# Optimization experiments

Measured on AMD Instinct MI355X. Metric: run time of the kernel, lower is better.

## Reference

```python
import jax, jax.numpy as jnp
import numpy as np

# Hyperparameters mirroring init_kwargs
MAX_ITERS = 100      # ADMM outer iterations
RHO = 1.0            # ADMM penalty
INNER = 20           # PGD steps per x-subproblem
STEP = 5e-05         # fixed PGD step (x_inner_step given, so no svdvals branch)


def setup_inputs() -> dict:
    key = jax.random.key(0)
    kA, kb, kc = jax.random.split(key, 3)
    m, n = 2048, 4096
    A = jax.random.normal(kA, (m, n), dtype=jnp.float32)
    b = jax.random.uniform(kb, (m,), dtype=jnp.float32)
    c = jax.random.uniform(kc, (n,), dtype=jnp.float32)
    return {"A": A, "b": b, "c": c}


def _admm(A, b, c):
    m, n = A.shape

    def outer(carry, _):
        x, s, u = carry
        r = s + b - u  # target for the x-subproblem residual

        # PGD on: min_{x>=0} c^T x + (rho/2)||A x - r||^2
        def pgd(x, _):
            g = c + RHO * (A.T @ (A @ x - r))
            return jnp.maximum(x - STEP * g, 0.0), None

        x, _ = jax.lax.scan(pgd, x, None, length=INNER)

        Ax = A @ x
        s = jnp.maximum(Ax - b + u, 0.0)   # slack update (projection onto >=0)
        u = u + (Ax - s - b)               # scaled dual update
        return (x, s, u), None

    init = (jnp.zeros((n,), A.dtype), jnp.zeros((m,), A.dtype), jnp.zeros((m,), A.dtype))
    (x, s, u), _ = jax.lax.scan(outer, init, None, length=MAX_ITERS)
    lambda_kkt = -RHO * u
    return x, s, u, lambda_kkt


def reference(A, b, c):
    # return_history=False -> torch module returns (x, s, u, lambda_kkt, None);
    # we return the 4 tensor outputs.
    return _admm(A, b, c)
```

## Files before the change

### kernel.cpp

```cpp
#include <hip/hip_runtime.h>
#include <hip/hip_cooperative_groups.h>

namespace cg = cooperative_groups;
typedef unsigned int u32;
typedef unsigned long long u64;

#define M_ROWS 2048
#define N_COLS 4096
#define RHO_C 1.0f
#define STEP_C 5e-05f
#define MAX_ITERS_C 100
#define INNER_C 20

__device__ __forceinline__ u64 ald64(const u64* p) {
    return __hip_atomic_load(p, __ATOMIC_RELAXED, __HIP_MEMORY_SCOPE_AGENT);
}
__device__ __forceinline__ void ast64(u64* p, u64 v) {
    __hip_atomic_store(p, v, __ATOMIC_RELAXED, __HIP_MEMORY_SCOPE_AGENT);
}
__device__ __forceinline__ void push_slot(u64* p, float v, u32 tag) {
    ast64(p, ((u64)tag << 32) | (u64)__float_as_uint(v));
}
__device__ __forceinline__ float4 poll4(const u64* p, u32 tag) {
    for (;;) {
        u64 a = ald64(p),     b = ald64(p + 1);
        u64 c = ald64(p + 2), d = ald64(p + 3);
        if (((u32)(a >> 32) == tag) & ((u32)(b >> 32) == tag) &
            ((u32)(c >> 32) == tag) & ((u32)(d >> 32) == tag))
            return make_float4(__uint_as_float((u32)a), __uint_as_float((u32)b),
                               __uint_as_float((u32)c), __uint_as_float((u32)d));
        __builtin_amdgcn_s_sleep(1);
    }
}
__device__ __forceinline__ float2 poll2(const u64* p, u32 tag) {
    for (;;) {
        u64 a = ald64(p), b = ald64(p + 1);
        if (((u32)(a >> 32) == tag) & ((u32)(b >> 32) == tag))
            return make_float2(__uint_as_float((u32)a), __uint_as_float((u32)b));
        __builtin_amdgcn_s_sleep(1);
    }
}

__global__ __launch_bounds__(1024) void admm_push(
    const float* __restrict__ A, const float* __restrict__ bvec,
    const float* __restrict__ cvec, float* __restrict__ out,
    u64* __restrict__ xmb, u64* __restrict__ rmb, int fanout)
{
    const int tid  = threadIdx.x;
    const int blk  = blockIdx.x;
    const int lane = tid & 63;
    const int wave = tid >> 6;
    const int cgp  = wave >> 2;
    const int rq   = wave & 3;
    const int cpy  = (fanout == 1) ? 0 : (blk & 7);

    __shared__ float  abuf[4 * N_COLS];
    __shared__ float4 xs4[1024];
    __shared__ float  red[4][16];
    __shared__ float4 gred[64];
    __shared__ float  wl[16], cw[16];
    __shared__ float  sv[8], uv[8], tpart[16], rtnew[8];

    float* xs = reinterpret_cast<float*>(xs4);
    const float4* A4 = reinterpret_cast<const float4*>(A);
    float4* abuf4 = reinterpret_cast<float4*>(abuf);
    const u64* xmyc = xmb + (size_t)cpy * 8192;
    const u64* rmyc = rmb + (size_t)cpy * 4096;

    if (tid < 16) cw[tid] = cvec[blk * 16 + tid];
    if (tid < 8) { sv[tid] = 0.0f; uv[tid] = 0.0f; }

    float accM[4][16];
    #pragma unroll
    for (int r = 0; r < 4; ++r)
        #pragma unroll
        for (int k = 0; k < 16; ++k) accM[r][k] = 0.0f;

    for (int i0 = 0; i0 < M_ROWS; i0 += 4) {
        #pragma unroll
        for (int ii = 0; ii < 4; ++ii)
            abuf4[ii * 1024 + tid] = A4[(size_t)(i0 + ii) * 1024 + tid];
        __syncthreads();
        #pragma unroll
        for (int ii = 0; ii < 4; ++ii) {
            const float*  row  = abuf + ii * N_COLS;
            const float4* row4 = abuf4 + ii * 1024;
            float4 av[4];
            #pragma unroll
            for (int q = 0; q < 4; ++q)
                av[q] = row4[256 * cgp + 64 * q + lane];
            float cb[4];
            #pragma unroll
            for (int r = 0; r < 4; ++r) cb[r] = row[blk * 16 + rq * 4 + r];
            #pragma unroll
            for (int r = 0; r < 4; ++r)
                #pragma unroll
                for (int q = 0; q < 4; ++q) {
                    accM[r][4*q+0] = fmaf(cb[r], av[q].x, accM[r][4*q+0]);
                    accM[r][4*q+1] = fmaf(cb[r], av[q].y, accM[r][4*q+1]);
                    accM[r][4*q+2] = fmaf(cb[r], av[q].z, accM[r][4*q+2]);
                    accM[r][4*q+3] = fmaf(cb[r], av[q].w, accM[r][4*q+3]);
                }
        }
        __syncthreads();
    }

    for (int outer = 0; outer < MAX_ITERS_C; ++outer) {
        if (outer == 0) {
            abuf[2 * tid]     = bvec[2 * tid];
            abuf[2 * tid + 1] = bvec[2 * tid + 1];
        } else {
            float2 rv = poll2(rmyc + (outer & 1) * 2048 + 2 * tid, (u32)outer);
            abuf[2 * tid]     = rv.x;
            abuf[2 * tid + 1] = rv.y;
        }
        __syncthreads();

        {
            const int p = tid >> 2, gq = tid & 3;
            float4 acc = {0.f, 0.f, 0.f, 0.f};
            #pragma unroll
            for (int k2 = 0; k2 < 8; ++k2) {
                const int i = p + 256 * k2;
                const float tv = abuf[i];
                float4 a = A4[(size_t)i * 1024 + blk * 4 + gq];
                acc.x = fmaf(a.x, tv, acc.x); acc.y = fmaf(a.y, tv, acc.y);
                acc.z = fmaf(a.z, tv, acc.z); acc.w = fmaf(a.w, tv, acc.w);
            }
            #pragma unroll
            for (int off = 4; off < 64; off <<= 1) {
                acc.x += __shfl_xor(acc.x, off);
                acc.y += __shfl_xor(acc.y, off);
                acc.z += __shfl_xor(acc.z, off);
                acc.w += __shfl_xor(acc.w, off);
            }
            if ((lane >> 2) == 0) gred[wave * 4 + gq] = acc;
        }
        __syncthreads();
        if (tid < 4) {
            float4 tot = {0.f, 0.f, 0.f, 0.f};
            #pragma unroll
            for (int w = 0; w < 16; ++w) {
                float4 v = gred[w * 4 + tid];
                tot.x += v.x; tot.y += v.y; tot.z += v.z; tot.w += v.w;
            }
            wl[tid * 4 + 0] = tot.x; wl[tid * 4 + 1] = tot.y;
            wl[tid * 4 + 2] = tot.z; wl[tid * 4 + 3] = tot.w;
        }
        __syncthreads();

        for (int inner = 0; inner < INNER_C; ++inner) {
            const u32 gs = (u32)(outer * INNER_C + inner);

            if (gs == 0) {
                xs4[tid] = make_float4(0.f, 0.f, 0.f, 0.f);
                __syncthreads();
            } else if (inner > 0) {
                float4 xv = poll4(xmyc + (gs & 1) * 4096 + 4 * tid, gs);
                __syncthreads();
                xs4[tid] = xv;
                __syncthreads();
            }

            float4 xq[4];
            #pragma unroll
            for (int q = 0; q < 4; ++q)
                xq[q] = xs4[256 * cgp + 64 * q + lane];

            float4 pd = {0.f, 0.f, 0.f, 0.f};
            #pragma unroll
            for (int q = 0; q < 4; ++q) {
                pd.x = fmaf(accM[0][4*q+0], xq[q].x, pd.x);
                pd.x = fmaf(accM[0][4*q+1], xq[q].y, pd.x);
                pd.x = fmaf(accM[0][4*q+2], xq[q].z, pd.x);
                pd.x = fmaf(accM[0][4*q+3], xq[q].w, pd.x);
                pd.y = fmaf(accM[1][4*q+0], xq[q].x, pd.y);
                pd.y = fmaf(accM[1][4*q+1], xq[q].y, pd.y);
                pd.y = fmaf(accM[1][4*q+2], xq[q].z, pd.y);
                pd.y = fmaf(accM[1][4*q+3], xq[q].w, pd.y);
                pd.z = fmaf(accM[2][4*q+0], xq[q].x, pd.z);
                pd.z = fmaf(accM[2][4*q+1], xq[q].y, pd.z);
                pd.z = fmaf(accM[2][4*q+2], xq[q].z, pd.z);
                pd.z = fmaf(accM[2][4*q+3], xq[q].w, pd.z);
                pd.w = fmaf(accM[3][4*q+0], xq[q].x, pd.w);
                pd.w = fmaf(accM[3][4*q+1], xq[q].y, pd.w);
                pd.w = fmaf(accM[3][4*q+2], xq[q].z, pd.w);
                pd.w = fmaf(accM[3][4*q+3], xq[q].w, pd.w);
            }
            #pragma unroll
            for (int off = 32; off; off >>= 1) {
                pd.x += __shfl_xor(pd.x, off);
                pd.y += __shfl_xor(pd.y, off);
                pd.z += __shfl_xor(pd.z, off);
                pd.w += __shfl_xor(pd.w, off);
            }
            if (lane == 0) {
                red[cgp][rq * 4 + 0] = pd.x;
                red[cgp][rq * 4 + 1] = pd.y;
                red[cgp][rq * 4 + 2] = pd.z;
                red[cgp][rq * 4 + 3] = pd.w;
            }
            __syncthreads();

            if (tid < fanout * 16) {
                const int dst = tid >> 4, jj = tid & 15;
                const float y = red[0][jj] + red[1][jj]
                              + red[2][jj] + red[3][jj];
                const float g = cw[jj] + RHO_C * (y - wl[jj]);
                float xn = xs[blk * 16 + jj] - STEP_C * g;
                xn = xn > 0.f ? xn : 0.f;
                push_slot(xmb + (size_t)dst * 8192 + ((gs + 1) & 1) * 4096
                              + blk * 16 + jj, xn, gs + 1);
            }
        }

        {
            const u32 gsf = (u32)((outer + 1) * INNER_C);
            float4 xv = poll4(xmyc + (gsf & 1) * 4096 + 4 * tid, gsf);
            __syncthreads();
            xs4[tid] = xv;
            __syncthreads();
        }
        {
            const int r = blk * 8 + (wave >> 1), h = wave & 1;
            const float4* Ar = A4 + (size_t)r * 1024 + h * 512;
            const float4* xh = xs4 + h * 512;
            float4 acc = {0.f, 0.f, 0.f, 0.f};
            #pragma unroll
            for (int it = 0; it < 8; ++it) {
                float4 a = Ar[it * 64 + lane], xv = xh[it * 64 + lane];
                acc.x = fmaf(a.x, xv.x, acc.x); acc.y = fmaf(a.y, xv.y, acc.y);
                acc.z = fmaf(a.z, xv.z, acc.z); acc.w = fmaf(a.w, xv.w, acc.w);
            }
            float d = acc.x + acc.y + acc.z + acc.w;
            #pragma unroll
            for (int off = 32; off; off >>= 1) d += __shfl_xor(d, off);
            if (lane == 0) tpart[wave] = d;
        }
        __syncthreads();
        if (tid < 8) {
            const int i = blk * 8 + tid;
            const float a  = tpart[2 * tid] + tpart[2 * tid + 1];
            const float bb = bvec[i];
            const float uu = uv[tid];
            float sn = a - bb + uu; sn = sn > 0.f ? sn : 0.f;
            const float un = uu + a - sn - bb;
            sv[tid] = sn; uv[tid] = un;
            rtnew[tid] = sn + bb - un;
        }
        __syncthreads();
        if (tid < fanout * 8) {
            const int dst = tid >> 3, jj = tid & 7;
            push_slot(rmb + (size_t)dst * 4096 + ((outer + 1) & 1) * 2048
                          + blk * 8 + jj, rtnew[jj], (u32)(outer + 1));
        }
    }

    if (tid < 16) out[blk * 16 + tid] = xs[blk * 16 + tid];
    if (tid < 8) {
        const int i = blk * 8 + tid;
        out[4096 + i] = sv[tid];
        out[6144 + i] = uv[tid];
        out[8192 + i] = -uv[tid];
    }
}

extern "C" void kernel_launch(void* const* d_in, const int* in_sizes, int n_in,
                              void* d_out, int out_size, void* d_ws, size_t ws_size,
                              hipStream_t stream) {
    const float* A    = (const float*)d_in[0];
    const float* bvec = (const float*)d_in[1];
    const float* cvec = (const float*)d_in[2];
    float* out = (float*)d_out;

    int fanout = (ws_size >= (size_t)(1 << 20)) ? 8 : 1;
    u64* xmb = (u64*)d_ws;
    u64* rmb = xmb + (size_t)fanout * 8192;

    void* args[] = { (void*)&A, (void*)&bvec, (void*)&cvec, (void*)&out,
                     (void*)&xmb, (void*)&rmb, (void*)&fanout };
    hipError_t err = hipLaunchCooperativeKernel((const void*)admm_push,
                               dim3(256), dim3(1024), args, 0, stream);
    (void)err;
}
```

Before: 11.43 ms.

## Read x directly from mailboxes into registers, skipping shared staging and barriers

Inner PGD steps now poll x straight from the global mailbox slots into registers in the exact layout each wave needs, instead of staging through shared memory with two barriers. Reads are spread across four mailbox copies to reduce contention. The reduction buffer is double-buffered by parity so one barrier per step is enough, and each block keeps its own x entry in a register. The cost is that each thread spins on several remote copies, and correctness now depends on the parity buffering being race-free.

```diff
diff --git a/kernel.cpp b/kernel.cpp
--- a/kernel.cpp
+++ b/kernel.cpp
@@ -1,7 +1,5 @@
 #include <hip/hip_runtime.h>
-#include <hip/hip_cooperative_groups.h>
-
-namespace cg = cooperative_groups;
+
 typedef unsigned int u32;
 typedef unsigned long long u64;
 
@@ -20,6 +18,27 @@
 }
 __device__ __forceinline__ void push_slot(u64* p, float v, u32 tag) {
     ast64(p, ((u64)tag << 32) | (u64)__float_as_uint(v));
+}
+__device__ __forceinline__ void poll4x2(const u64* p0, const u64* p1, u32 tag,
+                                        float4& a, float4& b) {
+    for (;;) {
+        u64 x0 = ald64(p0), x1 = ald64(p0 + 1),
+            x2 = ald64(p0 + 2), x3 = ald64(p0 + 3);
+        u64 y0 = ald64(p1), y1 = ald64(p1 + 1),
+            y2 = ald64(p1 + 2), y3 = ald64(p1 + 3);
+        bool ok = ((u32)(x0 >> 32) == tag) & ((u32)(x1 >> 32) == tag) &
+                  ((u32)(x2 >> 32) == tag) & ((u32)(x3 >> 32) == tag) &
+                  ((u32)(y0 >> 32) == tag) & ((u32)(y1 >> 32) == tag) &
+                  ((u32)(y2 >> 32) == tag) & ((u32)(y3 >> 32) == tag);
+        if (ok) {
+            a = make_float4(__uint_as_float((u32)x0), __uint_as_float((u32)x1),
+                            __uint_as_float((u32)x2), __uint_as_float((u32)x3));
+            b = make_float4(__uint_as_float((u32)y0), __uint_as_float((u32)y1),
+                            __uint_as_float((u32)y2), __uint_as_float((u32)y3));
+            return;
+        }
+        __builtin_amdgcn_s_sleep(1);
+    }
 }
 __device__ __forceinline__ float4 poll4(const u64* p, u32 tag) {
     for (;;) {
@@ -41,7 +60,7 @@
     }
 }
 
-__global__ __launch_bounds__(1024) void admm_push(
+__global__ __launch_bounds__(1024) void admm_direct(
     const float* __restrict__ A, const float* __restrict__ bvec,
     const float* __restrict__ cvec, float* __restrict__ out,
     u64* __restrict__ xmb, u64* __restrict__ rmb, int fanout)
@@ -56,7 +75,7 @@
 
     __shared__ float  abuf[4 * N_COLS];
     __shared__ float4 xs4[1024];
-    __shared__ float  red[4][16];
+    __shared__ float  red[2][4][16];
     __shared__ float4 gred[64];
     __shared__ float  wl[16], cw[16];
     __shared__ float  sv[8], uv[8], tpart[16], rtnew[8];
@@ -64,8 +83,14 @@
     float* xs = reinterpret_cast<float*>(xs4);
     const float4* A4 = reinterpret_cast<const float4*>(A);
     float4* abuf4 = reinterpret_cast<float4*>(abuf);
-    const u64* xmyc = xmb + (size_t)cpy * 8192;
     const u64* rmyc = rmb + (size_t)cpy * 4096;
+
+    const int c0 = (fanout == 1) ? 0 : ((blk + 0) & 7);
+    const int c1 = (fanout == 1) ? 0 : ((blk + 1) & 7);
+    const int c2 = (fanout == 1) ? 0 : ((blk + 2) & 7);
+    const int c3 = (fanout == 1) ? 0 : ((blk + 3) & 7);
+
+    float xold = 0.0f;
 
     if (tid < 16) cw[tid] = cvec[blk * 16 + tid];
     if (tid < 8) { sv[tid] = 0.0f; uv[tid] = 0.0f; }
@@ -151,42 +176,41 @@
 
         for (int inner = 0; inner < INNER_C; ++inner) {
             const u32 gs = (u32)(outer * INNER_C + inner);
-
-            if (gs == 0) {
-                xs4[tid] = make_float4(0.f, 0.f, 0.f, 0.f);
-                __syncthreads();
-            } else if (inner > 0) {
-                float4 xv = poll4(xmyc + (gs & 1) * 4096 + 4 * tid, gs);
-                __syncthreads();
-                xs4[tid] = xv;
-                __syncthreads();
-            }
-
-            float4 xq[4];
-            #pragma unroll
-            for (int q = 0; q < 4; ++q)
-                xq[q] = xs4[256 * cgp + 64 * q + lane];
+            const int par = (int)(gs & 1);
 
             float4 pd = {0.f, 0.f, 0.f, 0.f};
-            #pragma unroll
-            for (int q = 0; q < 4; ++q) {
-                pd.x = fmaf(accM[0][4*q+0], xq[q].x, pd.x);
-                pd.x = fmaf(accM[0][4*q+1], xq[q].y, pd.x);
-                pd.x = fmaf(accM[0][4*q+2], xq[q].z, pd.x);
-                pd.x = fmaf(accM[0][4*q+3], xq[q].w, pd.x);
-                pd.y = fmaf(accM[1][4*q+0], xq[q].x, pd.y);
-                pd.y = fmaf(accM[1][4*q+1], xq[q].y, pd.y);
-                pd.y = fmaf(accM[1][4*q+2], xq[q].z, pd.y);
-                pd.y = fmaf(accM[1][4*q+3], xq[q].w, pd.y);
-                pd.z = fmaf(accM[2][4*q+0], xq[q].x, pd.z);
-                pd.z = fmaf(accM[2][4*q+1], xq[q].y, pd.z);
-                pd.z = fmaf(accM[2][4*q+2], xq[q].z, pd.z);
-                pd.z = fmaf(accM[2][4*q+3], xq[q].w, pd.z);
-                pd.w = fmaf(accM[3][4*q+0], xq[q].x, pd.w);
-                pd.w = fmaf(accM[3][4*q+1], xq[q].y, pd.w);
-                pd.w = fmaf(accM[3][4*q+2], xq[q].z, pd.w);
-                pd.w = fmaf(accM[3][4*q+3], xq[q].w, pd.w);
-            }
+            if (gs != 0) {
+                const int base = par * 4096 + 1024 * cgp + 4 * lane;
+                float4 xa, xb;
+                poll4x2(xmb + (size_t)c0 * 8192 + base,
+                        xmb + (size_t)c1 * 8192 + base + 256, gs, xa, xb);
+                #pragma unroll
+                for (int r = 0; r < 4; ++r) {
+                    pd[r] = fmaf(accM[r][0], xa.x, pd[r]);
+                    pd[r] = fmaf(accM[r][1], xa.y, pd[r]);
+                    pd[r] = fmaf(accM[r][2], xa.z, pd[r]);
+                    pd[r] = fmaf(accM[r][3], xa.w, pd[r]);
+                    pd[r] = fmaf(accM[r][4], xb.x, pd[r]);
+                    pd[r] = fmaf(accM[r][5], xb.y, pd[r]);
+                    pd[r] = fmaf(accM[r][6], xb.z, pd[r]);
+                    pd[r] = fmaf(accM[r][7], xb.w, pd[r]);
+                }
+                float4 xc, xd;
+                poll4x2(xmb + (size_t)c2 * 8192 + base + 512,
+                        xmb + (size_t)c3 * 8192 + base + 768, gs, xc, xd);
+                #pragma unroll
+                for (int r = 0; r < 4; ++r) {
+                    pd[r] = fmaf(accM[r][ 8], xc.x, pd[r]);
+                    pd[r] = fmaf(accM[r][ 9], xc.y, pd[r]);
+                    pd[r] = fmaf(accM[r][10], xc.z, pd[r]);
+                    pd[r] = fmaf(accM[r][11], xc.w, pd[r]);
+                    pd[r] = fmaf(accM[r][12], xd.x, pd[r]);
+                    pd[r] = fmaf(accM[r][13], xd.y, pd[r]);
+                    pd[r] = fmaf(accM[r][14], xd.z, pd[r]);
+                    pd[r] = fmaf(accM[r][15], xd.w, pd[r]);
+                }
+            }
+
             #pragma unroll
             for (int off = 32; off; off >>= 1) {
                 pd.x += __shfl_xor(pd.x, off);
@@ -195,20 +219,21 @@
                 pd.w += __shfl_xor(pd.w, off);
             }
             if (lane == 0) {
-                red[cgp][rq * 4 + 0] = pd.x;
-                red[cgp][rq * 4 + 1] = pd.y;
-                red[cgp][rq * 4 + 2] = pd.z;
-                red[cgp][rq * 4 + 3] = pd.w;
+                red[par][cgp][rq * 4 + 0] = pd.x;
+                red[par][cgp][rq * 4 + 1] = pd.y;
+                red[par][cgp][rq * 4 + 2] = pd.z;
+                red[par][cgp][rq * 4 + 3] = pd.w;
             }
             __syncthreads();
 
             if (tid < fanout * 16) {
                 const int dst = tid >> 4, jj = tid & 15;
-                const float y = red[0][jj] + red[1][jj]
-                              + red[2][jj] + red[3][jj];
+                const float y = red[par][0][jj] + red[par][1][jj]
+                              + red[par][2][jj] + red[par][3][jj];
                 const float g = cw[jj] + RHO_C * (y - wl[jj]);
-                float xn = xs[blk * 16 + jj] - STEP_C * g;
+                float xn = xold - STEP_C * g;
                 xn = xn > 0.f ? xn : 0.f;
+                xold = xn;
                 push_slot(xmb + (size_t)dst * 8192 + ((gs + 1) & 1) * 4096
                               + blk * 16 + jj, xn, gs + 1);
             }
@@ -216,8 +241,8 @@
 
         {
             const u32 gsf = (u32)((outer + 1) * INNER_C);
-            float4 xv = poll4(xmyc + (gsf & 1) * 4096 + 4 * tid, gsf);
-            __syncthreads();
+            float4 xv = poll4(xmb + (size_t)cpy * 8192 + (gsf & 1) * 4096
+                                  + 4 * tid, gsf);
             xs4[tid] = xv;
             __syncthreads();
         }
@@ -279,7 +304,7 @@
 
     void* args[] = { (void*)&A, (void*)&bvec, (void*)&cvec, (void*)&out,
                      (void*)&xmb, (void*)&rmb, (void*)&fanout };
-    hipError_t err = hipLaunchCooperativeKernel((const void*)admm_push,
+    hipError_t err = hipLaunchCooperativeKernel((const void*)admm_direct,
                                dim3(256), dim3(1024), args, 0, stream);
     (void)err;
 }
```

Measured after the change: 23.88 ms. 109% more time.
